# Kernel tuning notes

Hardware: AMD Instinct MI355X
Metric: run time of the kernel (lower is better)

## Reference

```python
import jax, jax.numpy as jnp
import numpy as np

B, T, F = 4096, 256, 20
VOCAB, EMB = 1281, 4
UNITS = (64, 32, 32, 32)


def setup_inputs() -> dict:
    key = jax.random.key(0)
    ks = jax.random.split(key, 16)
    feats = jax.random.normal(ks[0], (B, T, F), jnp.float32)
    ids = jax.random.randint(ks[1], (B, T), 0, VOCAB).astype(jnp.float32)
    input_tensor = feats.at[:, :, 1].set(ids)  # column 1 = org ids
    W_emb = jax.random.normal(ks[2], (VOCAB, EMB), jnp.float32) * 0.1
    in_dims = (F - 2 + 1 + EMB,) + UNITS[:-1]  # (23, 64, 32, 32)
    out = {"input_tensor": input_tensor, "W_emb": W_emb}
    for i, (din, u) in enumerate(zip(in_dims, UNITS)):
        out[f"k{i}"] = jax.random.normal(ks[3 + 3 * i], (din, 3 * u), jnp.float32) * 0.1
        out[f"rk{i}"] = jax.random.normal(ks[4 + 3 * i], (u, 3 * u), jnp.float32) * 0.1
        out[f"b{i}"] = jnp.zeros((2, 3 * u), jnp.float32)  # [input_bias, recurrent_bias] (reset_after)
    out["Wd"] = jax.random.normal(ks[15], (UNITS[-1], 2), jnp.float32) * 0.1
    out["bd"] = jnp.zeros((2,), jnp.float32)
    return out


def _gru(h, x, k, rk, b):
    # Keras GRUCell, reset_after=True (TF2 default)
    mx = x @ k + b[0]
    mh = h @ rk + b[1]
    xz, xr, xh = jnp.split(mx, 3, axis=-1)
    hz, hr, hh = jnp.split(mh, 3, axis=-1)
    z = jax.nn.sigmoid(xz + hz)
    r = jax.nn.sigmoid(xr + hr)
    hc = jnp.tanh(xh + r * hh)
    return z * h + (1.0 - z) * hc


def reference(input_tensor, W_emb, k0, rk0, b0, k1, rk1, b1, k2, rk2, b2, k3, rk3, b3, Wd, bd):
    f0 = input_tensor[:, :, :1]                      # [B,T,1]
    ids = input_tensor[:, :, 1].astype(jnp.int32)    # [B,T]
    rest = input_tensor[:, :, 2:]                    # [B,T,F-2]
    emb = W_emb[ids]                                 # [B,T,EMB]
    x = jnp.concatenate([f0, rest, emb], axis=-1)    # [B,T,F+3]
    xs = jnp.swapaxes(x, 0, 1)                       # [T,B,F+3]
    bsz = x.shape[0]
    h_init = tuple(jnp.zeros((bsz, u), x.dtype) for u in UNITS)
    layer_params = ((k0, rk0, b0), (k1, rk1, b1), (k2, rk2, b2), (k3, rk3, b3))

    def step(carry, xt):
        hs = []
        inp = xt
        for h, (k, rk, b) in zip(carry, layer_params):
            h = _gru(h, inp, k, rk, b)
            hs.append(h)
            inp = h
        return tuple(hs), None

    hs, _ = jax.lax.scan(step, h_init, xs)
    # return_sequences + [:, -1, :] == final hidden state of last layer
    logits = hs[-1] @ Wd + bd
    return jax.nn.softmax(logits, axis=-1)
```

## Files before the change

kernel.cpp:

```cpp
#include <hip/hip_runtime.h>


typedef __attribute__((ext_vector_type(8))) __bf16 bf16x8;
typedef __attribute__((ext_vector_type(4))) float f32x4;

#define TT 256
#define FF 20
#define BT 16
#define CH 64
#define SH0 72
#define SH1 40
#define XSTR 648
#define NTHR 768

__device__ __forceinline__ f32x4 mfma16(bf16x8 a, bf16x8 b, f32x4 c) {
  return __builtin_amdgcn_mfma_f32_16x16x32_bf16(a, b, c, 0, 0, 0);
}

__device__ __forceinline__ float sigm(float x) {
  return __builtin_amdgcn_rcpf(1.f + __builtin_amdgcn_exp2f(-1.44269504f * x));
}
__device__ __forceinline__ float tanh_(float x) {
  return __builtin_amdgcn_rcpf(1.f + __builtin_amdgcn_exp2f(-2.88539008f * x)) * 2.f - 1.f;
}

__device__ __forceinline__ bf16x8 bfragW(const float* W, int Kreal, int N,
                                         int ncol, int kbase) {
  bf16x8 r;
#pragma unroll
  for (int j = 0; j < 8; ++j) {
    int k = kbase + j;
    r[j] = (__bf16)(k < Kreal ? W[k * N + ncol] : 0.f);
  }
  return r;
}

extern "C" __global__ void __launch_bounds__(NTHR, 3)
gru4(const float* __restrict__ inp, const float* __restrict__ Wemb,
     const float* __restrict__ k0, const float* __restrict__ rk0, const float* __restrict__ b0,
     const float* __restrict__ k1, const float* __restrict__ rk1, const float* __restrict__ b1,
     const float* __restrict__ k2, const float* __restrict__ rk2, const float* __restrict__ b2,
     const float* __restrict__ k3, const float* __restrict__ rk3, const float* __restrict__ b3,
     const float* __restrict__ Wd, const float* __restrict__ bd,
     float* __restrict__ out)
{
  __shared__ __align__(16) __bf16 x_ch[CH * XSTR];
  __shared__ __align__(16) __bf16 h0_lds[2][BT * SH0];
  __shared__ __align__(16) __bf16 h1_lds[2][BT * SH1];
  __shared__ __align__(16) __bf16 h2_lds[2][BT * SH1];
  __shared__ __align__(16) __bf16 h3_lds[2][BT * SH1];
  __shared__ __align__(16) float h3f[BT * 32];

  const int tid  = threadIdx.x;
  const int lane = tid & 63;
  const int w    = tid >> 6;
  const int col  = lane & 15;
  const int kb   = (lane >> 4) * 8;
  const int rowq = (lane >> 4) * 4;
  const long bbase = (long)blockIdx.x * BT;
  const float* binp = inp + bbase * TT * FF;

  bf16x8 zf;
#pragma unroll
  for (int j = 0; j < 8; ++j) zf[j] = (__bf16)0.f;

  bf16x8 Wz0 = zf, Wz1 = zf, Wz2 = zf;
  bf16x8 Wr0 = zf, Wr1 = zf, Wr2 = zf;
  bf16x8 Wgx0 = zf, Wgx1 = zf, Wgx2 = zf;
  bf16x8 Wgh0 = zf, Wgh1 = zf, Wgh2 = zf;
  float bz = 0.f, br = 0.f, bxh = 0.f, bhh = 0.f;
  const __bf16 *A0b = x_ch, *A1b = x_ch, *A2b = x_ch;
  int D0 = 0, D1 = 0, D2 = 0;
  __bf16* Wwr0 = (__bf16*)h3f;
  int WD = 0, wstride = SH1;
  int lay = 0;
  bool doLo = false, doHi = false, threeA = false;

  if (w < 6) {
    lay = 0; threeA = true;
    const int sl = (w < 4) ? (w >> 1) : (w - 2);
    doLo = (w >= 4) || ((w & 1) == 0);
    doHi = (w >= 4) || ((w & 1) == 1);
    const int u = sl * 16 + col;
    Wz0 = bfragW(k0, 23, 192, u, kb);
    Wz1 = bfragW(rk0, 64, 192, u, kb);
    Wz2 = bfragW(rk0, 64, 192, u, 32 + kb);
    Wr0 = bfragW(k0, 23, 192, 64 + u, kb);
    Wr1 = bfragW(rk0, 64, 192, 64 + u, kb);
    Wr2 = bfragW(rk0, 64, 192, 64 + u, 32 + kb);
    Wgx0 = bfragW(k0, 23, 192, 128 + u, kb);
    Wgh1 = bfragW(rk0, 64, 192, 128 + u, kb);
    Wgh2 = bfragW(rk0, 64, 192, 128 + u, 32 + kb);
    bz  = b0[u] + b0[192 + u];
    br  = b0[64 + u] + b0[192 + 64 + u];
    bxh = b0[128 + u];
    bhh = b0[192 + 128 + u];
    A1b = &h0_lds[0][col * SH0 + kb];      D1 = BT * SH0;
    A2b = &h0_lds[0][col * SH0 + 32 + kb]; D2 = BT * SH0;
    Wwr0 = &h0_lds[0][rowq * SH0 + sl * 16 + col];
    WD = BT * SH0; wstride = SH0;
  } else if (w < 8) {
    lay = 1; threeA = true; doLo = doHi = true;
    const int u = (w - 6) * 16 + col;
    Wz0 = bfragW(k1, 64, 96, u, kb);
    Wz1 = bfragW(k1, 64, 96, u, 32 + kb);
    Wz2 = bfragW(rk1, 32, 96, u, kb);
    Wr0 = bfragW(k1, 64, 96, 32 + u, kb);
    Wr1 = bfragW(k1, 64, 96, 32 + u, 32 + kb);
    Wr2 = bfragW(rk1, 32, 96, 32 + u, kb);
    Wgx0 = bfragW(k1, 64, 96, 64 + u, kb);
    Wgx1 = bfragW(k1, 64, 96, 64 + u, 32 + kb);
    Wgh2 = bfragW(rk1, 32, 96, 64 + u, kb);
    bz  = b1[u] + b1[96 + u];
    br  = b1[32 + u] + b1[96 + 32 + u];
    bxh = b1[64 + u];
    bhh = b1[96 + 64 + u];
    A0b = &h0_lds[0][col * SH0 + kb];      D0 = BT * SH0;
    A1b = &h0_lds[0][col * SH0 + 32 + kb]; D1 = BT * SH0;
    A2b = &h1_lds[0][col * SH1 + kb];      D2 = BT * SH1;
    Wwr0 = &h1_lds[0][rowq * SH1 + (w - 6) * 16 + col];
    WD = BT * SH1; wstride = SH1;
  } else if (w < 10) {
    lay = 2; threeA = false; doLo = doHi = true;
    const int u = (w - 8) * 16 + col;
    Wz0 = bfragW(k2, 32, 96, u, kb);
    Wz1 = bfragW(rk2, 32, 96, u, kb);
    Wr0 = bfragW(k2, 32, 96, 32 + u, kb);
    Wr1 = bfragW(rk2, 32, 96, 32 + u, kb);
    Wgx0 = bfragW(k2, 32, 96, 64 + u, kb);
    Wgh1 = bfragW(rk2, 32, 96, 64 + u, kb);
    bz  = b2[u] + b2[96 + u];
    br  = b2[32 + u] + b2[96 + 32 + u];
    bxh = b2[64 + u];
    bhh = b2[96 + 64 + u];
    A0b = &h1_lds[0][col * SH1 + kb]; D0 = BT * SH1;
    A1b = &h2_lds[0][col * SH1 + kb]; D1 = BT * SH1;
    A2b = A1b; D2 = D1;
    Wwr0 = &h2_lds[0][rowq * SH1 + (w - 8) * 16 + col];
    WD = BT * SH1; wstride = SH1;
  } else {
    lay = 3; threeA = false; doLo = doHi = true;
    const int u = (w - 10) * 16 + col;
    Wz0 = bfragW(k3, 32, 96, u, kb);
    Wz1 = bfragW(rk3, 32, 96, u, kb);
    Wr0 = bfragW(k3, 32, 96, 32 + u, kb);
    Wr1 = bfragW(rk3, 32, 96, 32 + u, kb);
    Wgx0 = bfragW(k3, 32, 96, 64 + u, kb);
    Wgh1 = bfragW(rk3, 32, 96, 64 + u, kb);
    bz  = b3[u] + b3[96 + u];
    br  = b3[32 + u] + b3[96 + 32 + u];
    bxh = b3[64 + u];
    bhh = b3[96 + 64 + u];
    A0b = &h2_lds[0][col * SH1 + kb]; D0 = BT * SH1;
    A1b = &h3_lds[0][col * SH1 + kb]; D1 = BT * SH1;
    A2b = A1b; D2 = D1;
    Wwr0 = &h3_lds[0][rowq * SH1 + (w - 10) * 16 + col];
    WD = BT * SH1; wstride = SH1;
  }

  const __bf16* xb = &x_ch[col * 40 + kb];

  {
    __bf16* p0 = (__bf16*)h0_lds;
    for (int i = tid; i < 2 * BT * SH0; i += NTHR) p0[i] = (__bf16)0.f;
    __bf16* p1 = (__bf16*)h1_lds;
    __bf16* p2 = (__bf16*)h2_lds;
    __bf16* p3 = (__bf16*)h3_lds;
    for (int i = tid; i < 2 * BT * SH1; i += NTHR) {
      p1[i] = (__bf16)0.f; p2[i] = (__bf16)0.f; p3[i] = (__bf16)0.f;
    }
  }
  float hreg[4] = {0.f, 0.f, 0.f, 0.f};
  __syncthreads();

  for (int s = 0; s < TT + 3; ++s) {
    if ((s & (CH - 1)) == 0 && s < TT) {
      for (int idx = tid; idx < BT * CH; idx += NTHR) {
        const int row = idx >> 6;
        const int tg  = idx & (CH - 1);
        const float* p = binp + ((long)row * TT + s + tg) * FF;
        float4 v0 = *(const float4*)(p);
        float4 v1 = *(const float4*)(p + 4);
        float4 v2 = *(const float4*)(p + 8);
        float4 v3 = *(const float4*)(p + 12);
        float4 v4 = *(const float4*)(p + 16);
        float4 e  = *(const float4*)(Wemb + 4 * (int)v0.y);
        __bf16* d = &x_ch[tg * XSTR + row * 40];
        bf16x8 q0 = {(__bf16)v0.x, (__bf16)v0.z, (__bf16)v0.w, (__bf16)v1.x,
                     (__bf16)v1.y, (__bf16)v1.z, (__bf16)v1.w, (__bf16)v2.x};
        bf16x8 q1 = {(__bf16)v2.y, (__bf16)v2.z, (__bf16)v2.w, (__bf16)v3.x,
                     (__bf16)v3.y, (__bf16)v3.z, (__bf16)v3.w, (__bf16)v4.x};
        bf16x8 q2 = {(__bf16)v4.y, (__bf16)v4.z, (__bf16)v4.w, (__bf16)e.x,
                     (__bf16)e.y,  (__bf16)e.z,  (__bf16)e.w,  (__bf16)0.f};
        *(bf16x8*)(d)      = q0;
        *(bf16x8*)(d + 8)  = q1;
        *(bf16x8*)(d + 16) = q2;
        *(bf16x8*)(d + 24) = zf;
      }
      __syncthreads();
    }

    const int pb = (s + 1) & 1;
    const int qb = s & 1;
    const int t  = s - lay;

    if (t >= 0 && t < TT) {
      const __bf16* a0p = (lay == 0) ? (xb + (s & (CH - 1)) * XSTR)
                                     : (A0b + pb * D0);
      bf16x8 A0 = *(const bf16x8*)a0p;
      bf16x8 A1 = *(const bf16x8*)(A1b + pb * D1);
      f32x4 az  = {bz, bz, bz, bz};
      f32x4 ar  = {br, br, br, br};
      f32x4 axh = {bxh, bxh, bxh, bxh};
      f32x4 ahh = {bhh, bhh, bhh, bhh};
      az  = mfma16(A0, Wz0, az);   az  = mfma16(A1, Wz1, az);
      ar  = mfma16(A0, Wr0, ar);   ar  = mfma16(A1, Wr1, ar);
      axh = mfma16(A0, Wgx0, axh); axh = mfma16(A1, Wgx1, axh);
      ahh = mfma16(A0, Wgh0, ahh); ahh = mfma16(A1, Wgh1, ahh);
      if (threeA) {
        bf16x8 A2 = *(const bf16x8*)(A2b + pb * D2);
        az  = mfma16(A2, Wz2, az);
        ar  = mfma16(A2, Wr2, ar);
        axh = mfma16(A2, Wgx2, axh);
        ahh = mfma16(A2, Wgh2, ahh);
      }
      __bf16* wr = Wwr0 + qb * WD;

#define GATE(r) { \
        float z  = sigm(az[r]); \
        float rg = sigm(ar[r]); \
        float hc = tanh_(fmaf(rg, ahh[r], axh[r])); \
        float hn = fmaf(z, hreg[r] - hc, hc); \
        hreg[r] = hn; \
        wr[(r) * wstride] = (__bf16)hn; }

      if (doLo) { GATE(0); GATE(1); }
      if (doHi) { GATE(2); GATE(3); }
#undef GATE
    }

    __syncthreads();
  }

  if (w >= 10) {
#pragma unroll
    for (int r = 0; r < 4; ++r)
      h3f[(rowq + r) * 32 + (w - 10) * 16 + col] = hreg[r];
  }
  __syncthreads();

  if (tid < BT) {
    float l0 = bd[0], l1 = bd[1];
#pragma unroll
    for (int u = 0; u < 32; ++u) {
      float h = h3f[tid * 32 + u];
      l0 = fmaf(h, Wd[2 * u], l0);
      l1 = fmaf(h, Wd[2 * u + 1], l1);
    }
    float m = fmaxf(l0, l1);
    float e0 = __builtin_amdgcn_exp2f((l0 - m) * 1.44269504f);
    float e1 = __builtin_amdgcn_exp2f((l1 - m) * 1.44269504f);
    float inv = 1.f / (e0 + e1);
    out[(bbase + tid) * 2 + 0] = e0 * inv;
    out[(bbase + tid) * 2 + 1] = e1 * inv;
  }
}

extern "C" void kernel_launch(void* const* d_in, const int* in_sizes, int n_in,
                              void* d_out, int out_size, void* d_ws, size_t ws_size,
                              hipStream_t stream) {
  const float* inp  = (const float*)d_in[0];
  const float* Wemb = (const float*)d_in[1];
  const float* k0   = (const float*)d_in[2];
  const float* rk0  = (const float*)d_in[3];
  const float* b0   = (const float*)d_in[4];
  const float* k1   = (const float*)d_in[5];
  const float* rk1  = (const float*)d_in[6];
  const float* b1   = (const float*)d_in[7];
  const float* k2   = (const float*)d_in[8];
  const float* rk2  = (const float*)d_in[9];
  const float* b2   = (const float*)d_in[10];
  const float* k3   = (const float*)d_in[11];
  const float* rk3  = (const float*)d_in[12];
  const float* b3   = (const float*)d_in[13];
  const float* Wd   = (const float*)d_in[14];
  const float* bd   = (const float*)d_in[15];
  float* out = (float*)d_out;

  const int Btot = in_sizes[0] / (TT * FF);
  dim3 grid(Btot / BT);
  gru4<<<grid, NTHR, 0, stream>>>(inp, Wemb, k0, rk0, b0, k1, rk1, b1,
                                  k2, rk2, b2, k3, rk3, b3, Wd, bd, out);
}
```

Before: 345.5 us.

## Grow block to 16 waves, split layer 0 and 1 gate work across wave pairs

Raises the block from 12 to 16 wavefronts. Layer 0 now uses 8 waves, each pair sharing a unit slice and splitting the gate rows into low and high halves. Layer 1 now uses 4 waves split the same way, which shortens the per-step critical path of the two heaviest layers. Bias vectors are hoisted out of the loop and the MFMA chains are interleaved. The cost is more waves per block, which may cut resident blocks per CU and adds barrier participants.

```diff
diff --git a/kernel.cpp b/kernel.cpp
--- a/kernel.cpp
+++ b/kernel.cpp
@@ -11,7 +11,7 @@
 #define SH0 72
 #define SH1 40
 #define XSTR 648
-#define NTHR 768
+#define NTHR 1024
 
 __device__ __forceinline__ f32x4 mfma16(bf16x8 a, bf16x8 b, f32x4 c) {
   return __builtin_amdgcn_mfma_f32_16x16x32_bf16(a, b, c, 0, 0, 0);
@@ -35,7 +35,7 @@
   return r;
 }
 
-extern "C" __global__ void __launch_bounds__(NTHR, 3)
+extern "C" __global__ void __launch_bounds__(NTHR, 4)
 gru4(const float* __restrict__ inp, const float* __restrict__ Wemb,
      const float* __restrict__ k0, const float* __restrict__ rk0, const float* __restrict__ b0,
      const float* __restrict__ k1, const float* __restrict__ rk1, const float* __restrict__ b1,
@@ -76,11 +76,11 @@
   int lay = 0;
   bool doLo = false, doHi = false, threeA = false;
 
-  if (w < 6) {
+  if (w < 8) {
     lay = 0; threeA = true;
-    const int sl = (w < 4) ? (w >> 1) : (w - 2);
-    doLo = (w >= 4) || ((w & 1) == 0);
-    doHi = (w >= 4) || ((w & 1) == 1);
+    const int sl = w >> 1;
+    doLo = ((w & 1) == 0);
+    doHi = ((w & 1) == 1);
     const int u = sl * 16 + col;
     Wz0 = bfragW(k0, 23, 192, u, kb);
     Wz1 = bfragW(rk0, 64, 192, u, kb);
@@ -99,9 +99,12 @@
     A2b = &h0_lds[0][col * SH0 + 32 + kb]; D2 = BT * SH0;
     Wwr0 = &h0_lds[0][rowq * SH0 + sl * 16 + col];
     WD = BT * SH0; wstride = SH0;
-  } else if (w < 8) {
-    lay = 1; threeA = true; doLo = doHi = true;
-    const int u = (w - 6) * 16 + col;
+  } else if (w < 12) {
+    lay = 1; threeA = true;
+    const int sl = (w - 8) >> 1;
+    doLo = ((w & 1) == 0);
+    doHi = ((w & 1) == 1);
+    const int u = sl * 16 + col;
     Wz0 = bfragW(k1, 64, 96, u, kb);
     Wz1 = bfragW(k1, 64, 96, u, 32 + kb);
     Wz2 = bfragW(rk1, 32, 96, u, kb);
@@ -118,11 +121,11 @@
     A0b = &h0_lds[0][col * SH0 + kb];      D0 = BT * SH0;
     A1b = &h0_lds[0][col * SH0 + 32 + kb]; D1 = BT * SH0;
     A2b = &h1_lds[0][col * SH1 + kb];      D2 = BT * SH1;
-    Wwr0 = &h1_lds[0][rowq * SH1 + (w - 6) * 16 + col];
+    Wwr0 = &h1_lds[0][rowq * SH1 + sl * 16 + col];
     WD = BT * SH1; wstride = SH1;
-  } else if (w < 10) {
+  } else if (w < 14) {
     lay = 2; threeA = false; doLo = doHi = true;
-    const int u = (w - 8) * 16 + col;
+    const int u = (w - 12) * 16 + col;
     Wz0 = bfragW(k2, 32, 96, u, kb);
     Wz1 = bfragW(rk2, 32, 96, u, kb);
     Wr0 = bfragW(k2, 32, 96, 32 + u, kb);
@@ -136,11 +139,11 @@
     A0b = &h1_lds[0][col * SH1 + kb]; D0 = BT * SH1;
     A1b = &h2_lds[0][col * SH1 + kb]; D1 = BT * SH1;
     A2b = A1b; D2 = D1;
-    Wwr0 = &h2_lds[0][rowq * SH1 + (w - 8) * 16 + col];
+    Wwr0 = &h2_lds[0][rowq * SH1 + (w - 12) * 16 + col];
     WD = BT * SH1; wstride = SH1;
   } else {
     lay = 3; threeA = false; doLo = doHi = true;
-    const int u = (w - 10) * 16 + col;
+    const int u = (w - 14) * 16 + col;
     Wz0 = bfragW(k3, 32, 96, u, kb);
     Wz1 = bfragW(rk3, 32, 96, u, kb);
     Wr0 = bfragW(k3, 32, 96, 32 + u, kb);
@@ -154,9 +157,14 @@
     A0b = &h2_lds[0][col * SH1 + kb]; D0 = BT * SH1;
     A1b = &h3_lds[0][col * SH1 + kb]; D1 = BT * SH1;
     A2b = A1b; D2 = D1;
-    Wwr0 = &h3_lds[0][rowq * SH1 + (w - 10) * 16 + col];
+    Wwr0 = &h3_lds[0][rowq * SH1 + (w - 14) * 16 + col];
     WD = BT * SH1; wstride = SH1;
   }
+
+  const f32x4 BZ  = {bz, bz, bz, bz};
+  const f32x4 BR  = {br, br, br, br};
+  const f32x4 BXH = {bxh, bxh, bxh, bxh};
+  const f32x4 BHH = {bhh, bhh, bhh, bhh};
 
   const __bf16* xb = &x_ch[col * 40 + kb];
 
@@ -172,6 +180,14 @@
   }
   float hreg[4] = {0.f, 0.f, 0.f, 0.f};
   __syncthreads();
+
+#define GATE(r) { \
+    float z  = sigm(az[r]); \
+    float rg = sigm(ar[r]); \
+    float hc = tanh_(fmaf(rg, ahh[r], axh[r])); \
+    float hn = fmaf(z, hreg[r] - hc, hc); \
+    hreg[r] = hn; \
+    wr[(r) * wstride] = (__bf16)hn; }
 
   for (int s = 0; s < TT + 3; ++s) {
     if ((s & (CH - 1)) == 0 && s < TT) {
@@ -209,14 +225,14 @@
                                      : (A0b + pb * D0);
       bf16x8 A0 = *(const bf16x8*)a0p;
       bf16x8 A1 = *(const bf16x8*)(A1b + pb * D1);
-      f32x4 az  = {bz, bz, bz, bz};
-      f32x4 ar  = {br, br, br, br};
-      f32x4 axh = {bxh, bxh, bxh, bxh};
-      f32x4 ahh = {bhh, bhh, bhh, bhh};
-      az  = mfma16(A0, Wz0, az);   az  = mfma16(A1, Wz1, az);
-      ar  = mfma16(A0, Wr0, ar);   ar  = mfma16(A1, Wr1, ar);
-      axh = mfma16(A0, Wgx0, axh); axh = mfma16(A1, Wgx1, axh);
-      ahh = mfma16(A0, Wgh0, ahh); ahh = mfma16(A1, Wgh1, ahh);
+      f32x4 az  = mfma16(A0, Wz0, BZ);
+      f32x4 ar  = mfma16(A0, Wr0, BR);
+      f32x4 axh = mfma16(A0, Wgx0, BXH);
+      f32x4 ahh = mfma16(A0, Wgh0, BHH);
+      az  = mfma16(A1, Wz1, az);
+      ar  = mfma16(A1, Wr1, ar);
+      axh = mfma16(A1, Wgx1, axh);
+      ahh = mfma16(A1, Wgh1, ahh);
       if (threeA) {
         bf16x8 A2 = *(const bf16x8*)(A2b + pb * D2);
         az  = mfma16(A2, Wz2, az);
@@ -226,26 +242,18 @@
       }
       __bf16* wr = Wwr0 + qb * WD;
 
-#define GATE(r) { \
-        float z  = sigm(az[r]); \
-        float rg = sigm(ar[r]); \
-        float hc = tanh_(fmaf(rg, ahh[r], axh[r])); \
-        float hn = fmaf(z, hreg[r] - hc, hc); \
-        hreg[r] = hn; \
-        wr[(r) * wstride] = (__bf16)hn; }
-
       if (doLo) { GATE(0); GATE(1); }
       if (doHi) { GATE(2); GATE(3); }
+    }
+
+    __syncthreads();
+  }
 #undef GATE
-    }
-
-    __syncthreads();
-  }
-
-  if (w >= 10) {
+
+  if (w >= 14) {
 #pragma unroll
     for (int r = 0; r < 4; ++r)
-      h3f[(rowq + r) * 32 + (w - 10) * 16 + col] = hreg[r];
+      h3f[(rowq + r) * 32 + (w - 14) * 16 + col] = hreg[r];
   }
   __syncthreads();
 
```

Measured after the change: 358.1 us. 3.7% more time.
